# Kernel optimization log

Hardware: AMD Instinct MI355X
Metric: run time of the kernel (lower is better)

The kernel has to match this reference:

```python
import jax, jax.numpy as jnp
import numpy as np

B, S, D = 8, 2048, 512
H, DK, DV = 8, 64, 64


def setup_inputs() -> dict:
    key = jax.random.key(0)
    ks = jax.random.split(key, 12)
    def xavier(k, shape):
        fan_in, fan_out = shape[0], shape[1]
        std = (2.0 / (fan_in + fan_out)) ** 0.5
        return jax.random.normal(k, shape, dtype=jnp.float32) * std
    return {
        "Q": jax.random.normal(ks[0], (B, S, D), dtype=jnp.float32),
        "K": jax.random.normal(ks[1], (B, S, D), dtype=jnp.float32),
        "V": jax.random.normal(ks[2], (B, S, D), dtype=jnp.float32),
        "W_q": xavier(ks[3], (D, H * DK)),
        "W_k": xavier(ks[4], (D, H * DK)),
        "W_v": xavier(ks[5], (D, H * DV)),
        "W_o": xavier(ks[6], (H * DV, D)),
        "W1": xavier(ks[7], (D, D)),  # linear1.weight, stored [out, in]
        "b1": jnp.zeros((D,), dtype=jnp.float32),
        "W2": xavier(ks[8], (D, D)),  # linear2.weight
        "b2": jnp.zeros((D,), dtype=jnp.float32),
    }


def reference(Q, K, V, W_q, W_k, W_v, W_o, W1, b1, W2, b2):
    eps = 1e-6
    bsz, q_len, _ = Q.shape
    # project and split heads: [B, S, H, dk]
    Qh = (Q @ W_q).reshape(bsz, q_len, H, DK)
    Kh = (K @ W_k).reshape(bsz, q_len, H, DK)
    Vh = (V @ W_v).reshape(bsz, q_len, H, DV)
    temperature = DK ** 0.5
    # scores: [B, H, Sq, Sk] (full O(N^2) matrix, as in original)
    scores = jnp.einsum('bqhd,bkhd->bhqk', Qh, Kh) / (temperature + eps)
    probs = jax.nn.softmax(scores, axis=-1)  # dropout = identity (eval)
    V_att = jnp.einsum('bhqk,bkhd->bqhd', probs, Vh).reshape(bsz, q_len, H * DV)
    attn_out = V_att @ W_o  # dropout = identity
    X = Q + attn_out
    # FFN: linear2(relu(linear1(X))); torch Linear: x @ W.T + b
    ffn = jax.nn.relu(X @ W1.T + b1) @ W2.T + b2
    return ffn + X
```

## Files before the change

### kernel.cpp

```cpp
#include <hip/hip_runtime.h>
#include <stdint.h>

typedef __bf16 bf16;
typedef bf16 bf16x8 __attribute__((ext_vector_type(8)));
typedef bf16 bf16x4 __attribute__((ext_vector_type(4)));
typedef float f32x2 __attribute__((ext_vector_type(2)));
typedef float f32x4 __attribute__((ext_vector_type(4)));
typedef float f32x16 __attribute__((ext_vector_type(16)));

#define AS1 __attribute__((address_space(1)))
#define AS3 __attribute__((address_space(3)))

__device__ __forceinline__ void gll16(const void* g, void* l) {
    __builtin_amdgcn_global_load_lds((const AS1 unsigned int*)g,
                                     (AS3 unsigned int*)l, 16, 0, 0);
}

__device__ __forceinline__ bf16 f2bf(float x) { return (bf16)x; }

__device__ __forceinline__ float fexp2(float x) { return __builtin_amdgcn_exp2f(x); }

#define QSCALE_LOG2E 0.18033685757f

__global__ void k_castqkv(const float* __restrict__ Q, const float* __restrict__ K,
                          const float* __restrict__ V,
                          bf16* __restrict__ oq, bf16* __restrict__ ok, bf16* __restrict__ ov)
{
    const int z = blockIdx.y;
    const float* in = z == 0 ? Q : z == 1 ? K : V;
    bf16* out = z == 0 ? oq : z == 1 ? ok : ov;
    const int i = blockIdx.x * 256 + threadIdx.x;
    for (size_t j = (size_t)i * 4; j < 8388608u; j += (size_t)2048 * 256 * 4) {
        float4 v = *(const float4*)(in + j);
        bf16x4 o;
        o[0] = f2bf(v.x); o[1] = f2bf(v.y); o[2] = f2bf(v.z); o[3] = f2bf(v.w);
        *(bf16x4*)(out + j) = o;
    }
}

__global__ void k_castw(const float* __restrict__ Wq, const float* __restrict__ Wk,
                        const float* __restrict__ Wv, const float* __restrict__ Wo,
                        const float* __restrict__ W1, const float* __restrict__ W2,
                        bf16* __restrict__ oq, bf16* __restrict__ ok, bf16* __restrict__ ov,
                        bf16* __restrict__ oo, bf16* __restrict__ o1, bf16* __restrict__ o2)
{
    const int z = blockIdx.y;
    const int idx = blockIdx.x * 256 + threadIdx.x;
    const float* src = z == 0 ? Wq : z == 1 ? Wk : z == 2 ? Wv : z == 3 ? Wo : z == 4 ? W1 : W2;
    bf16* dst = z == 0 ? oq : z == 1 ? ok : z == 2 ? ov : z == 3 ? oo : z == 4 ? o1 : o2;
    if (z < 4) {
        const int n = idx >> 9, k = idx & 511;
        dst[idx] = f2bf(src[(k << 9) + n]);
    } else {
        dst[idx] = f2bf(src[idx]);
    }
}

__device__ __forceinline__ void gemm_core(const bf16* __restrict__ A,
                                          const bf16* __restrict__ Bt,
                                          const int K, bf16* As, bf16* Bs,
                                          const int bm, const int bn,
                                          f32x4 acc[4][4])
{
    const int tid  = threadIdx.x;
    const int lane = tid & 63;
    const int wave = tid >> 6;
    const int g    = lane >> 4;
    const int l15  = lane & 15;
    const int wm   = (wave >> 1) * 64;
    const int wn   = (wave & 1) * 64;

    const int srow = tid >> 2;
    const int sk   = (tid & 3) * 8;
    const size_t aoff0 = (size_t)(bm + srow) * K + sk;
    const size_t aoff1 = (size_t)(bm + 64 + srow) * K + sk;
    const size_t boff0 = (size_t)(bn + srow) * K + sk;
    const size_t boff1 = (size_t)(bn + 64 + srow) * K + sk;
    char* asb = (char*)As + wave * 1024;
    char* bsb = (char*)Bs + wave * 1024;

    for (int kt = 0; kt < K; kt += 32) {
        __syncthreads();
        gll16(A + aoff0 + kt, asb);
        gll16(A + aoff1 + kt, asb + 4096);
        gll16(Bt + boff0 + kt, bsb);
        gll16(Bt + boff1 + kt, bsb + 4096);
        __syncthreads();
        bf16x8 af[4], bfv[4];
#pragma unroll
        for (int mi = 0; mi < 4; ++mi)
            af[mi] = *(const bf16x8*)&As[(wm + mi * 16 + l15) * 32 + g * 8];
#pragma unroll
        for (int ni = 0; ni < 4; ++ni)
            bfv[ni] = *(const bf16x8*)&Bs[(wn + ni * 16 + l15) * 32 + g * 8];
#pragma unroll
        for (int mi = 0; mi < 4; ++mi)
#pragma unroll
            for (int ni = 0; ni < 4; ++ni)
                acc[mi][ni] = __builtin_amdgcn_mfma_f32_16x16x32_bf16(
                    af[mi], bfv[ni], acc[mi][ni], 0, 0, 0);
    }
}

template<int EPI>
__global__ __launch_bounds__(256)
void k_gemm(const bf16* __restrict__ A, const bf16* __restrict__ Bt,
            const float* __restrict__ bias,
            const bf16* __restrict__ residb,
            float* __restrict__ Cf, bf16* __restrict__ Cb,
            int M, int N, int K)
{
    __shared__ bf16 As[128 * 32];
    __shared__ bf16 Bs[128 * 32];
    const int bm = blockIdx.y * 128, bn = blockIdx.x * 128;
    f32x4 acc[4][4] = {};
    gemm_core(A, Bt, K, As, Bs, bm, bn, acc);

    const int tid  = threadIdx.x;
    const int lane = tid & 63;
    const int wave = tid >> 6;
    const int g    = lane >> 4;
    const int l15  = lane & 15;
    const int wm   = (wave >> 1) * 64;
    const int wn   = (wave & 1) * 64;
    const int col0 = bn + wn + l15;
#pragma unroll
    for (int ni = 0; ni < 4; ++ni) {
        const int col = col0 + ni * 16;
        float bv = 0.f;
        if constexpr (EPI == 2 || EPI == 3) bv = bias[col];
#pragma unroll
        for (int mi = 0; mi < 4; ++mi) {
#pragma unroll
            for (int r = 0; r < 4; ++r) {
                const int row = bm + wm + mi * 16 + 4 * g + r;
                const size_t idx = (size_t)row * N + col;
                float v = acc[mi][ni][r];
                if constexpr (EPI == 1) {
                    Cb[idx] = f2bf(v + (float)residb[idx]);
                } else if constexpr (EPI == 2) {
                    Cb[idx] = f2bf(fmaxf(v + bv, 0.f));
                } else {
                    Cf[idx] = v + bv + (float)residb[idx];
                }
            }
        }
    }
}

__global__ __launch_bounds__(256)
void k_proj(const bf16* __restrict__ Qb, const bf16* __restrict__ Kb, const bf16* __restrict__ Vb,
            const bf16* __restrict__ BQ, const bf16* __restrict__ BK, const bf16* __restrict__ BV,
            bf16* __restrict__ OQ, bf16* __restrict__ OK_, bf16* __restrict__ OV)
{
    __shared__ bf16 SM[8192];
    const int z = blockIdx.z;
    const bf16* A  = z == 0 ? Qb : z == 1 ? Kb : Vb;
    const bf16* Bt = z == 0 ? BQ : z == 1 ? BK : BV;
    bf16* Cb       = z == 0 ? OQ : z == 1 ? OK_ : OV;
    const int bm = blockIdx.y * 128, bn = blockIdx.x * 128;
    f32x4 acc[4][4] = {};
    gemm_core(A, Bt, 512, SM, SM + 4096, bm, bn, acc);

    const int tid  = threadIdx.x;
    const int lane = tid & 63;
    const int wave = tid >> 6;
    const int g    = lane >> 4;
    const int l15  = lane & 15;
    const int wn   = (wave & 1) * 64;
    const int bb   = bm >> 11;
    const int s0   = bm & 2047;

    __syncthreads();
#pragma unroll
    for (int p = 0; p < 2; ++p) {
        if ((wave >> 1) == p) {
            if (z == 0) {
#pragma unroll
                for (int ni = 0; ni < 4; ++ni) {
                    const int col = wn + ni * 16 + l15;
                    const int hh = col >> 6, dk = col & 63;
                    char* img = (char*)SM + hh * 8192;
#pragma unroll
                    for (int mi = 0; mi < 4; ++mi)
#pragma unroll
                        for (int r = 0; r < 4; ++r) {
                            const int sl = mi * 16 + 4 * g + r;
                            *(bf16*)(img + (sl * 64 + dk) * 2) =
                                f2bf(acc[mi][ni][r] * QSCALE_LOG2E);
                        }
                }
            } else if (z == 1) {
#pragma unroll
                for (int ni = 0; ni < 4; ++ni) {
                    const int col = wn + ni * 16 + l15;
                    const int hh = col >> 6, dk = col & 63;
                    const int ks = dk >> 4, h2 = (dk >> 3) & 1, e = dk & 7;
                    char* img = (char*)SM + hh * 8192;
#pragma unroll
                    for (int mi = 0; mi < 4; ++mi)
#pragma unroll
                        for (int r = 0; r < 4; ++r) {
                            const int sl = mi * 16 + 4 * g + r;
                            const int t2 = sl >> 5, ql = sl & 31;
                            const int off = (((t2 * 4 + ks) * 64 + h2 * 32 + ql) * 8 + e) * 2;
                            *(bf16*)(img + off) = f2bf(acc[mi][ni][r]);
                        }
                }
            } else {
#pragma unroll
                for (int ni = 0; ni < 4; ++ni) {
                    const int col = wn + ni * 16 + l15;
                    const int hh = col >> 6, dv = col & 63;
                    const int dvt = dv >> 5, ql = dv & 31;
                    char* img = (char*)SM + hh * 8192;
#pragma unroll
                    for (int mi = 0; mi < 4; ++mi)
#pragma unroll
                        for (int r = 0; r < 4; ++r) {
                            const int sl = mi * 16 + 4 * g + r;
                            const int kt = sl >> 4, kk = sl & 15;
                            const int h2 = (kk >> 2) & 1;
                            const int e = (kk & 3) | ((kk >> 3) << 2);
                            const int off = (((dvt * 4 + kt) * 64 + h2 * 32 + ql) * 8 + e) * 2;
                            *(bf16*)(img + off) = f2bf(acc[mi][ni][r]);
                        }
                }
            }
        }
        __syncthreads();
        {
            const int hh = tid >> 7, t = tid & 127;
            const int hg = (bn >> 6) + hh;
            const size_t a0 = (size_t)(bb * 8 + hg) * 131072;
            const size_t slab = (z == 0) ? a0 + (size_t)(s0 + p * 64) * 64
                                         : a0 + (size_t)((s0 >> 6) + p) * 4096;
            const char* img = (const char*)SM + hh * 8192;
#pragma unroll
            for (int i = 0; i < 4; ++i) {
                const int G = i * 128 + t;
                bf16x8 vv = *(const bf16x8*)(img + G * 16);
                *(bf16x8*)&Cb[slab + (size_t)G * 8] = vv;
            }
        }
        if (p == 0) __syncthreads();
    }
}

__global__ __launch_bounds__(256, 4)
void k_attn(const bf16* __restrict__ Qp, const bf16* __restrict__ Khp,
            const bf16* __restrict__ Vtp, bf16* __restrict__ O)
{
    __shared__ bf16 smem[16384];
    const int tid = threadIdx.x;
    const int l   = tid & 63;
    const int w   = tid >> 6;
    const int h   = l >> 5;
    const int ql  = l & 31;
    const int d   = blockIdx.x;
    const int bh  = ((d >> 7) << 3) | (d & 7);
    const int qt  = (d >> 3) & 15;
    const size_t base = (size_t)bh * 131072;
    const int q0 = qt * 128 + w * 32;
    const int loff = l * 16;

    bf16x8 qf[4];
#pragma unroll
    for (int ks = 0; ks < 4; ++ks)
        qf[ks] = *(const bf16x8*)&Qp[base + (size_t)(q0 + ql) * 64 + ks * 16 + h * 8];

    f32x16 o0 = {}, o1 = {};
    float lrun = 0.f;

    const bf16* ksrc = Khp + base + tid * 8;
    const bf16* vsrc = Vtp + base + tid * 8;
    char* kb0 = (char*)smem;
    char* kb1 = (char*)smem + 16384;
    const int wdst = w * 1024;

    auto stage = [&](int kvt, char* kb) {
        const bf16* ks = ksrc + kvt * 4096;
        const bf16* vs = vsrc + kvt * 4096;
        gll16(ks,        kb + wdst);
        gll16(ks + 2048, kb + 4096 + wdst);
        gll16(vs,        kb + 8192 + wdst);
        gll16(vs + 2048, kb + 12288 + wdst);
    };

    auto compute = [&](const char* kb) {
        f32x16 s0 = {}, s1 = {};
        __builtin_amdgcn_s_setprio(1);
#pragma unroll
        for (int ks = 0; ks < 4; ++ks) {
            bf16x8 a0 = *(const bf16x8*)(kb + ks * 1024 + loff);
            bf16x8 a1 = *(const bf16x8*)(kb + 4096 + ks * 1024 + loff);
            s0 = __builtin_amdgcn_mfma_f32_32x32x16_bf16(a0, qf[ks], s0, 0, 0, 0);
            s1 = __builtin_amdgcn_mfma_f32_32x32x16_bf16(a1, qf[ks], s1, 0, 0, 0);
        }
        __builtin_amdgcn_s_setprio(0);

        f32x2 pA = {0.f, 0.f}, pB = {0.f, 0.f};
#pragma unroll
        for (int r = 0; r < 16; r += 2) {
            s0[r]     = fexp2(s0[r]);
            s0[r + 1] = fexp2(s0[r + 1]);
            s1[r]     = fexp2(s1[r]);
            s1[r + 1] = fexp2(s1[r + 1]);
            pA += (f32x2){s0[r], s0[r + 1]};
            pB += (f32x2){s1[r], s1[r + 1]};
        }
        const f32x2 pC = pA + pB;
        lrun += pC[0] + pC[1];

        bf16x8 pb[4];
#pragma unroll
        for (int j = 0; j < 4; ++j) {
            const int ofs = 8 * (j & 1);
#pragma unroll
            for (int e = 0; e < 8; ++e)
                pb[j][e] = f2bf((j & 2) ? s1[ofs + e] : s0[ofs + e]);
        }

        const char* vr = kb + 8192;
        __builtin_amdgcn_s_setprio(1);
#pragma unroll
        for (int j = 0; j < 4; ++j) {
            bf16x8 a0 = *(const bf16x8*)(vr + j * 1024 + loff);
            bf16x8 a1 = *(const bf16x8*)(vr + 4096 + j * 1024 + loff);
            o0 = __builtin_amdgcn_mfma_f32_32x32x16_bf16(a0, pb[j], o0, 0, 0, 0);
            o1 = __builtin_amdgcn_mfma_f32_32x32x16_bf16(a1, pb[j], o1, 0, 0, 0);
        }
        __builtin_amdgcn_s_setprio(0);
    };

    stage(0, kb0);
    __syncthreads();
    for (int kvt = 0; kvt < 32; kvt += 2) {
        if (kvt + 1 < 32) stage(kvt + 1, kb1);
        compute(kb0);
        __syncthreads();
        if (kvt + 2 < 32) stage(kvt + 2, kb0);
        compute(kb1);
        __syncthreads();
    }

    lrun += __shfl_xor(lrun, 32);
    const float inv = 1.f / lrun;

    char* ot = (char*)smem + w * 4096;
#pragma unroll
    for (int dvt = 0; dvt < 2; ++dvt) {
#pragma unroll
        for (int r = 0; r < 16; ++r) {
            const int dv = dvt * 32 + (r & 3) + 8 * (r >> 2) + 4 * h;
            const float val = (dvt ? o1[r] : o0[r]) * inv;
            *(bf16*)(ot + ql * 128 + ((((dv >> 3) ^ (ql & 7)) << 4) | ((dv & 7) << 1))) = f2bf(val);
        }
    }
    const int qr = l >> 1;
    const int dh4 = (l & 1) * 4;
    const size_t ob = ((size_t)(bh >> 3) * 2048 + q0 + qr) * 512 + (bh & 7) * 64 + (size_t)dh4 * 8;
#pragma unroll
    for (int B = 0; B < 4; ++B) {
        bf16x8 v = *(const bf16x8*)(ot + qr * 128 + (((dh4 + B) ^ (qr & 7)) << 4));
        *(bf16x8*)&O[ob + B * 8] = v;
    }
}

extern "C" void kernel_launch(void* const* d_in, const int* in_sizes, int n_in,
                              void* d_out, int out_size, void* d_ws, size_t ws_size,
                              hipStream_t stream)
{
    const float* Q  = (const float*)d_in[0];
    const float* K  = (const float*)d_in[1];
    const float* V  = (const float*)d_in[2];
    const float* Wq = (const float*)d_in[3];
    const float* Wk = (const float*)d_in[4];
    const float* Wv = (const float*)d_in[5];
    const float* Wo = (const float*)d_in[6];
    const float* W1 = (const float*)d_in[7];
    const float* b1 = (const float*)d_in[8];
    const float* W2 = (const float*)d_in[9];
    const float* b2 = (const float*)d_in[10];
    float* out = (float*)d_out;

    const int M = 8 * 2048;
    const size_t TN = (size_t)M * 512;
    const int WN = 512 * 512;

    char* ws = (char*)d_ws;
    bf16* Qbf  = (bf16*)ws;
    bf16* Kbf  = Qbf + TN;
    bf16* Vbf  = Kbf + TN;
    bf16* Qhp  = Vbf + TN;
    bf16* Khp  = Qhp + TN;
    bf16* Vtp  = Khp + TN;
    bf16* Vatt = Vtp + TN;
    bf16* H1   = Vatt + TN;
    bf16* Wqt  = H1 + TN;
    bf16* Wkt  = Wqt + WN;
    bf16* Wvt  = Wkt + WN;
    bf16* Wot  = Wvt + WN;
    bf16* W1b  = Wot + WN;
    bf16* W2b  = W1b + WN;
    bf16* Xbf  = Vbf;

    k_castqkv<<<dim3(2048, 3), 256, 0, stream>>>(Q, K, V, Qbf, Kbf, Vbf);
    k_castw<<<dim3(1024, 6), 256, 0, stream>>>(Wq, Wk, Wv, Wo, W1, W2,
                                               Wqt, Wkt, Wvt, Wot, W1b, W2b);

    k_proj<<<dim3(4, 128, 3), 256, 0, stream>>>(Qbf, Kbf, Vbf, Wqt, Wkt, Wvt,
                                                Qhp, Khp, Vtp);

    k_attn<<<1024, 256, 0, stream>>>(Qhp, Khp, Vtp, Vatt);

    dim3 gg(4, 128);
    k_gemm<1><<<gg, 256, 0, stream>>>(Vatt, Wot, nullptr, Qbf, nullptr, Xbf, M, 512, 512);
    k_gemm<2><<<gg, 256, 0, stream>>>(Xbf, W1b, b1, nullptr, nullptr, H1, M, 512, 512);
    k_gemm<3><<<gg, 256, 0, stream>>>(H1, W2b, b2, Xbf, out, nullptr, M, 512, 512);
}
```

Measured before the change: 220.2 us.

## Process two 32-query tiles per wave in attention to reuse K/V fragments

Each wave in the attention kernel now handles 64 query rows, as two 32-row MFMA tiles, instead of 32. Every K and V fragment read from LDS is fed to two MFMAs, which halves LDS traffic and staging per unit of work. The grid shrinks from 1024 to 512 blocks and launch bounds drop to 2 blocks per CU to make room for the doubled accumulators. In exchange, register pressure rises and fewer waves are resident to hide latency, with only 2 blocks per CU across the device.

```diff
diff --git a/kernel.cpp b/kernel.cpp
--- a/kernel.cpp
+++ b/kernel.cpp
@@ -247,7 +247,7 @@
     }
 }
 
-__global__ __launch_bounds__(256, 4)
+__global__ __launch_bounds__(256, 2)
 void k_attn(const bf16* __restrict__ Qp, const bf16* __restrict__ Khp,
             const bf16* __restrict__ Vtp, bf16* __restrict__ O)
 {
@@ -258,19 +258,21 @@
     const int h   = l >> 5;
     const int ql  = l & 31;
     const int d   = blockIdx.x;
-    const int bh  = ((d >> 7) << 3) | (d & 7);
-    const int qt  = (d >> 3) & 15;
+    const int bh  = ((d >> 6) << 3) | (d & 7);
+    const int qt  = (d >> 3) & 7;
     const size_t base = (size_t)bh * 131072;
-    const int q0 = qt * 128 + w * 32;
+    const int q0 = qt * 256 + w * 64;
     const int loff = l * 16;
 
-    bf16x8 qf[4];
-#pragma unroll
-    for (int ks = 0; ks < 4; ++ks)
-        qf[ks] = *(const bf16x8*)&Qp[base + (size_t)(q0 + ql) * 64 + ks * 16 + h * 8];
-
-    f32x16 o0 = {}, o1 = {};
-    float lrun = 0.f;
+    bf16x8 qfA[4], qfB[4];
+#pragma unroll
+    for (int ks = 0; ks < 4; ++ks) {
+        qfA[ks] = *(const bf16x8*)&Qp[base + (size_t)(q0 + ql) * 64 + ks * 16 + h * 8];
+        qfB[ks] = *(const bf16x8*)&Qp[base + (size_t)(q0 + 32 + ql) * 64 + ks * 16 + h * 8];
+    }
+
+    f32x16 oA0 = {}, oA1 = {}, oB0 = {}, oB1 = {};
+    float lrunA = 0.f, lrunB = 0.f;
 
     const bf16* ksrc = Khp + base + tid * 8;
     const bf16* vsrc = Vtp + base + tid * 8;
@@ -288,37 +290,50 @@
     };
 
     auto compute = [&](const char* kb) {
-        f32x16 s0 = {}, s1 = {};
+        f32x16 sA0 = {}, sA1 = {}, sB0 = {}, sB1 = {};
         __builtin_amdgcn_s_setprio(1);
 #pragma unroll
         for (int ks = 0; ks < 4; ++ks) {
             bf16x8 a0 = *(const bf16x8*)(kb + ks * 1024 + loff);
             bf16x8 a1 = *(const bf16x8*)(kb + 4096 + ks * 1024 + loff);
-            s0 = __builtin_amdgcn_mfma_f32_32x32x16_bf16(a0, qf[ks], s0, 0, 0, 0);
-            s1 = __builtin_amdgcn_mfma_f32_32x32x16_bf16(a1, qf[ks], s1, 0, 0, 0);
+            sA0 = __builtin_amdgcn_mfma_f32_32x32x16_bf16(a0, qfA[ks], sA0, 0, 0, 0);
+            sB0 = __builtin_amdgcn_mfma_f32_32x32x16_bf16(a0, qfB[ks], sB0, 0, 0, 0);
+            sA1 = __builtin_amdgcn_mfma_f32_32x32x16_bf16(a1, qfA[ks], sA1, 0, 0, 0);
+            sB1 = __builtin_amdgcn_mfma_f32_32x32x16_bf16(a1, qfB[ks], sB1, 0, 0, 0);
         }
         __builtin_amdgcn_s_setprio(0);
 
         f32x2 pA = {0.f, 0.f}, pB = {0.f, 0.f};
 #pragma unroll
         for (int r = 0; r < 16; r += 2) {
-            s0[r]     = fexp2(s0[r]);
-            s0[r + 1] = fexp2(s0[r + 1]);
-            s1[r]     = fexp2(s1[r]);
-            s1[r + 1] = fexp2(s1[r + 1]);
-            pA += (f32x2){s0[r], s0[r + 1]};
-            pB += (f32x2){s1[r], s1[r + 1]};
-        }
-        const f32x2 pC = pA + pB;
-        lrun += pC[0] + pC[1];
-
-        bf16x8 pb[4];
+            sA0[r]     = fexp2(sA0[r]);
+            sA0[r + 1] = fexp2(sA0[r + 1]);
+            sA1[r]     = fexp2(sA1[r]);
+            sA1[r + 1] = fexp2(sA1[r + 1]);
+            pA += (f32x2){sA0[r], sA0[r + 1]};
+            pA += (f32x2){sA1[r], sA1[r + 1]};
+        }
+#pragma unroll
+        for (int r = 0; r < 16; r += 2) {
+            sB0[r]     = fexp2(sB0[r]);
+            sB0[r + 1] = fexp2(sB0[r + 1]);
+            sB1[r]     = fexp2(sB1[r]);
+            sB1[r + 1] = fexp2(sB1[r + 1]);
+            pB += (f32x2){sB0[r], sB0[r + 1]};
+            pB += (f32x2){sB1[r], sB1[r + 1]};
+        }
+        lrunA += pA[0] + pA[1];
+        lrunB += pB[0] + pB[1];
+
+        bf16x8 pbA[4], pbB[4];
 #pragma unroll
         for (int j = 0; j < 4; ++j) {
             const int ofs = 8 * (j & 1);
 #pragma unroll
-            for (int e = 0; e < 8; ++e)
-                pb[j][e] = f2bf((j & 2) ? s1[ofs + e] : s0[ofs + e]);
+            for (int e = 0; e < 8; ++e) {
+                pbA[j][e] = f2bf((j & 2) ? sA1[ofs + e] : sA0[ofs + e]);
+                pbB[j][e] = f2bf((j & 2) ? sB1[ofs + e] : sB0[ofs + e]);
+            }
         }
 
         const char* vr = kb + 8192;
@@ -327,8 +342,10 @@
         for (int j = 0; j < 4; ++j) {
             bf16x8 a0 = *(const bf16x8*)(vr + j * 1024 + loff);
             bf16x8 a1 = *(const bf16x8*)(vr + 4096 + j * 1024 + loff);
-            o0 = __builtin_amdgcn_mfma_f32_32x32x16_bf16(a0, pb[j], o0, 0, 0, 0);
-            o1 = __builtin_amdgcn_mfma_f32_32x32x16_bf16(a1, pb[j], o1, 0, 0, 0);
+            oA0 = __builtin_amdgcn_mfma_f32_32x32x16_bf16(a0, pbA[j], oA0, 0, 0, 0);
+            oB0 = __builtin_amdgcn_mfma_f32_32x32x16_bf16(a0, pbB[j], oB0, 0, 0, 0);
+            oA1 = __builtin_amdgcn_mfma_f32_32x32x16_bf16(a1, pbA[j], oA1, 0, 0, 0);
+            oB1 = __builtin_amdgcn_mfma_f32_32x32x16_bf16(a1, pbB[j], oB1, 0, 0, 0);
         }
         __builtin_amdgcn_s_setprio(0);
     };
@@ -344,27 +361,30 @@
         __syncthreads();
     }
 
-    lrun += __shfl_xor(lrun, 32);
-    const float inv = 1.f / lrun;
-
     char* ot = (char*)smem + w * 4096;
-#pragma unroll
-    for (int dvt = 0; dvt < 2; ++dvt) {
-#pragma unroll
-        for (int r = 0; r < 16; ++r) {
-            const int dv = dvt * 32 + (r & 3) + 8 * (r >> 2) + 4 * h;
-            const float val = (dvt ? o1[r] : o0[r]) * inv;
-            *(bf16*)(ot + ql * 128 + ((((dv >> 3) ^ (ql & 7)) << 4) | ((dv & 7) << 1))) = f2bf(val);
-        }
-    }
     const int qr = l >> 1;
     const int dh4 = (l & 1) * 4;
-    const size_t ob = ((size_t)(bh >> 3) * 2048 + q0 + qr) * 512 + (bh & 7) * 64 + (size_t)dh4 * 8;
-#pragma unroll
-    for (int B = 0; B < 4; ++B) {
-        bf16x8 v = *(const bf16x8*)(ot + qr * 128 + (((dh4 + B) ^ (qr & 7)) << 4));
-        *(bf16x8*)&O[ob + B * 8] = v;
-    }
+    auto epi = [&](const f32x16& e0, const f32x16& e1, float lr, int qg) {
+        lr += __shfl_xor(lr, 32);
+        const float inv = 1.f / lr;
+#pragma unroll
+        for (int dvt = 0; dvt < 2; ++dvt) {
+#pragma unroll
+            for (int r = 0; r < 16; ++r) {
+                const int dv = dvt * 32 + (r & 3) + 8 * (r >> 2) + 4 * h;
+                const float val = (dvt ? e1[r] : e0[r]) * inv;
+                *(bf16*)(ot + ql * 128 + ((((dv >> 3) ^ (ql & 7)) << 4) | ((dv & 7) << 1))) = f2bf(val);
+            }
+        }
+        const size_t ob = ((size_t)(bh >> 3) * 2048 + qg + qr) * 512 + (bh & 7) * 64 + (size_t)dh4 * 8;
+#pragma unroll
+        for (int B = 0; B < 4; ++B) {
+            bf16x8 v = *(const bf16x8*)(ot + qr * 128 + (((dh4 + B) ^ (qr & 7)) << 4));
+            *(bf16x8*)&O[ob + B * 8] = v;
+        }
+    };
+    epi(oA0, oA1, lrunA, q0);
+    epi(oB0, oB1, lrunB, q0 + 32);
 }
 
 extern "C" void kernel_launch(void* const* d_in, const int* in_sizes, int n_in,
@@ -412,7 +432,7 @@
     k_proj<<<dim3(4, 128, 3), 256, 0, stream>>>(Qbf, Kbf, Vbf, Wqt, Wkt, Wvt,
                                                 Qhp, Khp, Vtp);
 
-    k_attn<<<1024, 256, 0, stream>>>(Qhp, Khp, Vtp, Vatt);
+    k_attn<<<512, 256, 0, stream>>>(Qhp, Khp, Vtp, Vatt);
 
     dim3 gg(4, 128);
     k_gemm<1><<<gg, 256, 0, stream>>>(Vatt, Wot, nullptr, Qbf, nullptr, Xbf, M, 512, 512);
```

Measured after the change: 210.2 us. -4.5%, faster.
